# Optimization experiments

Hardware: AMD Instinct MI355X
Metric: run time of the kernel (lower is better)

## Reference

```python
import jax, jax.numpy as jnp
import numpy as np

N_POS = 8192
BATCH = 4
N_GT = 512
EPS = 1e-6
P_EXP = -1.0  # generalized-mean exponent (p < 0)


def setup_inputs() -> dict:
    key = jax.random.key(0)
    k1, k2, k3 = jax.random.split(key, 3)
    dis_matrix = jax.random.uniform(k1, (N_POS, N_POS), dtype=jnp.float32)
    prob_map = jax.random.uniform(k2, (BATCH, N_POS), dtype=jnp.float32)
    gt = jax.random.randint(k3, (BATCH, N_GT), 0, N_POS, dtype=jnp.int64 if jax.config.jax_enable_x64 else jnp.int32)
    return {"prob_map": prob_map, "gt": gt, "dis_matrix": dis_matrix}


def reference(prob_map, gt, dis_matrix):
    max_dist = jnp.max(dis_matrix)
    # global min-max normalization with detached min/range (matches torch .detach())
    pmin = jax.lax.stop_gradient(jnp.min(prob_map))
    prange = jax.lax.stop_gradient(jnp.max(prob_map) - jnp.min(prob_map))
    prob = jnp.clip((prob_map - pmin) / prange, 0.0, 1.0)  # (B, N)

    # gather gt-indexed columns: dis_matrix[:, gt] -> (N, B, G) -> (B, N, G)
    D = jnp.transpose(jnp.take(dis_matrix, gt, axis=1), (1, 0, 2))

    n_est = prob.sum(axis=1)  # (B,)
    # term 1: (1/n_est) * sum_n p_n * min_g D[n, g]
    term1 = jnp.sum(prob * jnp.min(D, axis=2), axis=1) / (n_est + EPS)  # (B,)

    # term 2: generalized mean over pixel dim of weighted distance matrix
    w = (1.0 - prob)[:, :, None] * max_dist + prob[:, :, None] * D  # (B, N, G)
    minn = jnp.mean((w + EPS) ** P_EXP, axis=1) ** (1.0 / P_EXP)  # (B, G)
    term2 = jnp.mean(minn, axis=1)  # (B,)

    return jnp.mean(term1) + jnp.mean(term2)
```

## Files before the change

### kernel.cpp

```cpp
#include <hip/hip_runtime.h>
#include <math.h>

#define N_POS 8192
#define BATCH 4
#define N_GT 512
#define BG 2048
#define EPSV 1e-6f

#define KA_BLOCKS 2048
#define ROWS_A 4
#define KC_BLOCKS 1024
#define ROWS_C 8
#define RG 32
#define CHUNKS_PER_RG (KC_BLOCKS / RG)

#define WS_DPACK 0
#define WS_PARTS (N_POS * BG)
#define WS_PARTS2 (WS_PARTS + KC_BLOCKS * BG)
#define WS_MIND  (WS_PARTS2 + RG * BG)
#define WS_MAXP  (WS_MIND + BATCH * N_POS)
#define WS_SC    (WS_MAXP + KA_BLOCKS)

__global__ __launch_bounds__(256) void whd_kA(const float* __restrict__ dis,
                                              const int* __restrict__ gt,
                                              float* __restrict__ wsf) {
    __shared__ float rowbuf[N_POS];
    __shared__ unsigned short gtl[BG];
    __shared__ float smax[4];
    const int t = threadIdx.x;
    const int wv = t >> 6, lane = t & 63;
    const int row0 = blockIdx.x * ROWS_A;
    float* dpack = wsf + WS_DPACK;
    float* minD = wsf + WS_MIND;

    for (int i = t; i < BG; i += 256) gtl[i] = (unsigned short)gt[i];
    __syncthreads();
    int c[8];
    #pragma unroll
    for (int k = 0; k < 8; k++) c[k] = gtl[8 * t + k];

    float tmax = -INFINITY;
    for (int r = 0; r < ROWS_A; r++) {
        const int n = row0 + r;
        if (r > 0) __syncthreads();
        const float4* src = (const float4*)(dis + (size_t)n * N_POS);
        float4* dstl = (float4*)rowbuf;
        #pragma unroll
        for (int j = 0; j < N_POS / 4 / 256; j++) {
            int i = t + 256 * j;
            float4 v = src[i];
            tmax = fmaxf(tmax, fmaxf(fmaxf(v.x, v.y), fmaxf(v.z, v.w)));
            dstl[i] = v;
        }
        __syncthreads();
        float g0 = rowbuf[c[0]], g1 = rowbuf[c[1]], g2 = rowbuf[c[2]], g3 = rowbuf[c[3]];
        float g4 = rowbuf[c[4]], g5 = rowbuf[c[5]], g6 = rowbuf[c[6]], g7 = rowbuf[c[7]];
        float4* dst = (float4*)(dpack + (size_t)n * BG + 8 * t);
        dst[0] = make_float4(g0, g1, g2, g3);
        dst[1] = make_float4(g4, g5, g6, g7);
        float m = fminf(fminf(fminf(g0, g1), fminf(g2, g3)),
                        fminf(fminf(g4, g5), fminf(g6, g7)));
        #pragma unroll
        for (int off = 32; off; off >>= 1) m = fminf(m, __shfl_xor(m, off, 64));
        if (lane == 0) minD[wv * N_POS + n] = m;
    }
    #pragma unroll
    for (int off = 32; off; off >>= 1) tmax = fmaxf(tmax, __shfl_down(tmax, off, 64));
    if (lane == 0) smax[wv] = tmax;
    __syncthreads();
    if (t == 0)
        wsf[WS_MAXP + blockIdx.x] = fmaxf(fmaxf(smax[0], smax[1]), fmaxf(smax[2], smax[3]));
}

__global__ __launch_bounds__(1024) void whd_kB(const float* __restrict__ prob,
                                               float* __restrict__ wsf) {
    __shared__ float red[1024];
    const int t = threadIdx.x;
    float m = -INFINITY;
    for (int i = t; i < KA_BLOCKS; i += 1024) m = fmaxf(m, wsf[WS_MAXP + i]);
    red[t] = m; __syncthreads();
    for (int s = 512; s; s >>= 1) { if (t < s) red[t] = fmaxf(red[t], red[t + s]); __syncthreads(); }
    float maxdist = red[0]; __syncthreads();
    float lmin = INFINITY, lmax = -INFINITY;
    for (int i = t; i < BATCH * N_POS; i += 1024) {
        float v = prob[i];
        lmin = fminf(lmin, v); lmax = fmaxf(lmax, v);
    }
    red[t] = lmin; __syncthreads();
    for (int s = 512; s; s >>= 1) { if (t < s) red[t] = fminf(red[t], red[t + s]); __syncthreads(); }
    float pmin = red[0]; __syncthreads();
    red[t] = lmax; __syncthreads();
    for (int s = 512; s; s >>= 1) { if (t < s) red[t] = fmaxf(red[t], red[t + s]); __syncthreads(); }
    float pmax = red[0]; __syncthreads();
    float invr = 1.0f / (pmax - pmin);
    const float* minD = wsf + WS_MIND;
    for (int b = 0; b < BATCH; b++) {
        float sp = 0.f, spm = 0.f;
        for (int i = t; i < N_POS; i += 1024) {
            float p = (prob[b * N_POS + i] - pmin) * invr;
            p = fminf(fmaxf(p, 0.f), 1.f);
            sp += p;
            spm += p * minD[b * N_POS + i];
        }
        red[t] = sp; __syncthreads();
        for (int s = 512; s; s >>= 1) { if (t < s) red[t] += red[t + s]; __syncthreads(); }
        if (t == 0) wsf[WS_SC + 3 + b] = red[0];
        __syncthreads();
        red[t] = spm; __syncthreads();
        for (int s = 512; s; s >>= 1) { if (t < s) red[t] += red[t + s]; __syncthreads(); }
        if (t == 0) wsf[WS_SC + 7 + b] = red[0];
        __syncthreads();
    }
    if (t == 0) {
        wsf[WS_SC + 0] = maxdist;
        wsf[WS_SC + 1] = pmin;
        wsf[WS_SC + 2] = pmax - pmin;
        wsf[WS_SC + 11] = 0.f;
    }
}

__global__ __launch_bounds__(256) void whd_kC(const float* __restrict__ prob,
                                              float* __restrict__ wsf) {
    const int t = threadIdx.x;
    const int wv = t >> 6;
    const int row0 = blockIdx.x * ROWS_C;
    const float* dpack = wsf + WS_DPACK;
    const float maxd = wsf[WS_SC + 0];
    const float pmin = wsf[WS_SC + 1];
    const float invr = 1.0f / wsf[WS_SC + 2];
    float acc[8];
    #pragma unroll
    for (int k = 0; k < 8; k++) acc[k] = 0.f;
    #pragma unroll
    for (int r = 0; r < ROWS_C; r++) {
        const int n = row0 + r;
        float p = (prob[wv * N_POS + n] - pmin) * invr;
        p = fminf(fmaxf(p, 0.f), 1.f);
        const float4* rp = (const float4*)(dpack + (size_t)n * BG + 8 * t);
        float4 v0 = rp[0], v1 = rp[1];
        acc[0] += 1.0f / (fmaf(p, v0.x - maxd, maxd) + EPSV);
        acc[1] += 1.0f / (fmaf(p, v0.y - maxd, maxd) + EPSV);
        acc[2] += 1.0f / (fmaf(p, v0.z - maxd, maxd) + EPSV);
        acc[3] += 1.0f / (fmaf(p, v0.w - maxd, maxd) + EPSV);
        acc[4] += 1.0f / (fmaf(p, v1.x - maxd, maxd) + EPSV);
        acc[5] += 1.0f / (fmaf(p, v1.y - maxd, maxd) + EPSV);
        acc[6] += 1.0f / (fmaf(p, v1.z - maxd, maxd) + EPSV);
        acc[7] += 1.0f / (fmaf(p, v1.w - maxd, maxd) + EPSV);
    }
    float4* op = (float4*)(wsf + WS_PARTS + (size_t)blockIdx.x * BG + 8 * t);
    op[0] = make_float4(acc[0], acc[1], acc[2], acc[3]);
    op[1] = make_float4(acc[4], acc[5], acc[6], acc[7]);
}

__global__ __launch_bounds__(256) void whd_kD1(float* __restrict__ wsf) {
    const int t = threadIdx.x;
    const int col = blockIdx.x * 256 + t;
    const int rg = blockIdx.y;
    const float* parts = wsf + WS_PARTS + (size_t)rg * CHUNKS_PER_RG * BG;
    float s = 0.f;
    #pragma unroll 8
    for (int ch = 0; ch < CHUNKS_PER_RG; ch++) s += parts[(size_t)ch * BG + col];
    wsf[WS_PARTS2 + (size_t)rg * BG + col] = s;
}

__global__ __launch_bounds__(256) void whd_kD2(float* __restrict__ wsf) {
    __shared__ float red[256];
    const int t = threadIdx.x;
    const int col = blockIdx.x * 256 + t;
    const float* p2 = wsf + WS_PARTS2;
    float s = 0.f;
    #pragma unroll
    for (int rg = 0; rg < RG; rg++) s += p2[(size_t)rg * BG + col];
    float val = (float)N_POS / s;
    red[t] = val; __syncthreads();
    for (int st = 128; st; st >>= 1) { if (t < st) red[t] += red[t + st]; __syncthreads(); }
    if (t == 0) atomicAdd(&wsf[WS_SC + 11], red[0]);
}

__global__ __launch_bounds__(64) void whd_kE(const float* __restrict__ wsf,
                                             float* __restrict__ out) {
    if (threadIdx.x == 0) {
        float term1 = 0.f;
        for (int b = 0; b < BATCH; b++)
            term1 += wsf[WS_SC + 7 + b] / (wsf[WS_SC + 3 + b] + EPSV);
        term1 *= (1.0f / BATCH);
        float term2 = wsf[WS_SC + 11] * (1.0f / BG);
        out[0] = term1 + term2;
    }
}

extern "C" void kernel_launch(void* const* d_in, const int* in_sizes, int n_in,
                              void* d_out, int out_size, void* d_ws, size_t ws_size,
                              hipStream_t stream) {
    const float* prob = (const float*)d_in[0];
    const int* gt = (const int*)d_in[1];
    const float* dis = (const float*)d_in[2];
    float* out = (float*)d_out;
    float* wsf = (float*)d_ws;

    whd_kA<<<KA_BLOCKS, 256, 0, stream>>>(dis, gt, wsf);
    whd_kB<<<1, 1024, 0, stream>>>(prob, wsf);
    whd_kC<<<KC_BLOCKS, 256, 0, stream>>>(prob, wsf);
    whd_kD1<<<dim3(BG / 256, RG), 256, 0, stream>>>(wsf);
    whd_kD2<<<BG / 256, 256, 0, stream>>>(wsf);
    whd_kE<<<1, 64, 0, stream>>>(wsf, out);
}
```

Baseline: 431.5 us.

## Prefetch rows in register, use wave-shuffle reductions, fuse final kernel

The gather kernel now handles 8 rows per block and prefetches the next distance row into registers with nontemporal loads while the current row is processed from shared memory. The scalar-stats kernel replaces shared-memory tree reductions with wave shuffles and vectorised loads. The final kernel is merged into the last reduction using a last-block-done atomic counter, and the packed reads in the accumulation kernel are made nontemporal. This targets latency in the memory-bound row pass and removes launch and barrier overhead, at the cost of more registers and half as many gather blocks.

```diff
diff --git a/kernel.cpp b/kernel.cpp
--- a/kernel.cpp
+++ b/kernel.cpp
@@ -7,8 +7,8 @@
 #define BG 2048
 #define EPSV 1e-6f
 
-#define KA_BLOCKS 2048
-#define ROWS_A 4
+#define KA_BLOCKS 1024
+#define ROWS_A 8
 #define KC_BLOCKS 1024
 #define ROWS_C 8
 #define RG 32
@@ -21,6 +21,8 @@
 #define WS_MAXP  (WS_MIND + BATCH * N_POS)
 #define WS_SC    (WS_MAXP + KA_BLOCKS)
 
+typedef __attribute__((ext_vector_type(4))) float f32x4;
+
 __global__ __launch_bounds__(256) void whd_kA(const float* __restrict__ dis,
                                               const int* __restrict__ gt,
                                               float* __restrict__ wsf) {
@@ -34,6 +36,13 @@
     float* minD = wsf + WS_MIND;
 
     for (int i = t; i < BG; i += 256) gtl[i] = (unsigned short)gt[i];
+
+    f32x4 pre[8];
+    {
+        const f32x4* src = (const f32x4*)(dis + (size_t)row0 * N_POS);
+        #pragma unroll
+        for (int j = 0; j < 8; j++) pre[j] = __builtin_nontemporal_load(src + t + 256 * j);
+    }
     __syncthreads();
     int c[8];
     #pragma unroll
@@ -42,27 +51,32 @@
     float tmax = -INFINITY;
     for (int r = 0; r < ROWS_A; r++) {
         const int n = row0 + r;
-        if (r > 0) __syncthreads();
-        const float4* src = (const float4*)(dis + (size_t)n * N_POS);
-        float4* dstl = (float4*)rowbuf;
-        #pragma unroll
-        for (int j = 0; j < N_POS / 4 / 256; j++) {
-            int i = t + 256 * j;
-            float4 v = src[i];
+        f32x4* dstl = (f32x4*)rowbuf;
+        #pragma unroll
+        for (int j = 0; j < 8; j++) {
+            f32x4 v = pre[j];
             tmax = fmaxf(tmax, fmaxf(fmaxf(v.x, v.y), fmaxf(v.z, v.w)));
-            dstl[i] = v;
+            dstl[t + 256 * j] = v;
+        }
+        if (r + 1 < ROWS_A) {
+            const f32x4* srcn = (const f32x4*)(dis + (size_t)(n + 1) * N_POS);
+            #pragma unroll
+            for (int j = 0; j < 8; j++) pre[j] = __builtin_nontemporal_load(srcn + t + 256 * j);
         }
         __syncthreads();
         float g0 = rowbuf[c[0]], g1 = rowbuf[c[1]], g2 = rowbuf[c[2]], g3 = rowbuf[c[3]];
         float g4 = rowbuf[c[4]], g5 = rowbuf[c[5]], g6 = rowbuf[c[6]], g7 = rowbuf[c[7]];
-        float4* dst = (float4*)(dpack + (size_t)n * BG + 8 * t);
-        dst[0] = make_float4(g0, g1, g2, g3);
-        dst[1] = make_float4(g4, g5, g6, g7);
+        f32x4* dst = (f32x4*)(dpack + (size_t)n * BG + 8 * t);
+        f32x4 pk0; pk0.x = g0; pk0.y = g1; pk0.z = g2; pk0.w = g3;
+        f32x4 pk1; pk1.x = g4; pk1.y = g5; pk1.z = g6; pk1.w = g7;
+        dst[0] = pk0;
+        dst[1] = pk1;
         float m = fminf(fminf(fminf(g0, g1), fminf(g2, g3)),
                         fminf(fminf(g4, g5), fminf(g6, g7)));
         #pragma unroll
         for (int off = 32; off; off >>= 1) m = fminf(m, __shfl_xor(m, off, 64));
         if (lane == 0) minD[wv * N_POS + n] = m;
+        if (r + 1 < ROWS_A) __syncthreads();
     }
     #pragma unroll
     for (int off = 32; off; off >>= 1) tmax = fmaxf(tmax, __shfl_down(tmax, off, 64));
@@ -74,48 +88,71 @@
 
 __global__ __launch_bounds__(1024) void whd_kB(const float* __restrict__ prob,
                                                float* __restrict__ wsf) {
-    __shared__ float red[1024];
-    const int t = threadIdx.x;
+    __shared__ float sA[16], sB[16], sC[16];
+    const int t = threadIdx.x, wv = t >> 6, lane = t & 63;
+
     float m = -INFINITY;
     for (int i = t; i < KA_BLOCKS; i += 1024) m = fmaxf(m, wsf[WS_MAXP + i]);
-    red[t] = m; __syncthreads();
-    for (int s = 512; s; s >>= 1) { if (t < s) red[t] = fmaxf(red[t], red[t + s]); __syncthreads(); }
-    float maxdist = red[0]; __syncthreads();
+    #pragma unroll
+    for (int off = 32; off; off >>= 1) m = fmaxf(m, __shfl_xor(m, off, 64));
+
     float lmin = INFINITY, lmax = -INFINITY;
-    for (int i = t; i < BATCH * N_POS; i += 1024) {
-        float v = prob[i];
-        lmin = fminf(lmin, v); lmax = fmaxf(lmax, v);
-    }
-    red[t] = lmin; __syncthreads();
-    for (int s = 512; s; s >>= 1) { if (t < s) red[t] = fminf(red[t], red[t + s]); __syncthreads(); }
-    float pmin = red[0]; __syncthreads();
-    red[t] = lmax; __syncthreads();
-    for (int s = 512; s; s >>= 1) { if (t < s) red[t] = fmaxf(red[t], red[t + s]); __syncthreads(); }
-    float pmax = red[0]; __syncthreads();
-    float invr = 1.0f / (pmax - pmin);
-    const float* minD = wsf + WS_MIND;
+    const f32x4* p4 = (const f32x4*)prob;
+    for (int i = t; i < BATCH * N_POS / 4; i += 1024) {
+        f32x4 v = p4[i];
+        lmin = fminf(fminf(lmin, fminf(v.x, v.y)), fminf(v.z, v.w));
+        lmax = fmaxf(fmaxf(lmax, fmaxf(v.x, v.y)), fmaxf(v.z, v.w));
+    }
+    #pragma unroll
+    for (int off = 32; off; off >>= 1) {
+        lmin = fminf(lmin, __shfl_xor(lmin, off, 64));
+        lmax = fmaxf(lmax, __shfl_xor(lmax, off, 64));
+    }
+    if (lane == 0) { sA[wv] = m; sB[wv] = lmin; sC[wv] = lmax; }
+    __syncthreads();
+    if (t == 0) {
+        float maxd = -INFINITY, mn = INFINITY, mx = -INFINITY;
+        #pragma unroll
+        for (int i = 0; i < 16; i++) {
+            maxd = fmaxf(maxd, sA[i]); mn = fminf(mn, sB[i]); mx = fmaxf(mx, sC[i]);
+        }
+        wsf[WS_SC + 0] = maxd;
+        wsf[WS_SC + 1] = mn;
+        wsf[WS_SC + 2] = mx - mn;
+        wsf[WS_SC + 11] = 0.f;
+        wsf[WS_SC + 12] = 0.f;
+        sB[0] = mn; sC[0] = 1.0f / (mx - mn);
+    }
+    __syncthreads();
+    const float pmin = sB[0], invr = sC[0];
+
+    const f32x4* d4 = (const f32x4*)(wsf + WS_MIND);
     for (int b = 0; b < BATCH; b++) {
         float sp = 0.f, spm = 0.f;
-        for (int i = t; i < N_POS; i += 1024) {
-            float p = (prob[b * N_POS + i] - pmin) * invr;
-            p = fminf(fmaxf(p, 0.f), 1.f);
-            sp += p;
-            spm += p * minD[b * N_POS + i];
-        }
-        red[t] = sp; __syncthreads();
-        for (int s = 512; s; s >>= 1) { if (t < s) red[t] += red[t + s]; __syncthreads(); }
-        if (t == 0) wsf[WS_SC + 3 + b] = red[0];
+        for (int i = t; i < N_POS / 4; i += 1024) {
+            f32x4 v = p4[b * (N_POS / 4) + i];
+            f32x4 dm = d4[b * (N_POS / 4) + i];
+            float p;
+            p = fminf(fmaxf((v.x - pmin) * invr, 0.f), 1.f); sp += p; spm += p * dm.x;
+            p = fminf(fmaxf((v.y - pmin) * invr, 0.f), 1.f); sp += p; spm += p * dm.y;
+            p = fminf(fmaxf((v.z - pmin) * invr, 0.f), 1.f); sp += p; spm += p * dm.z;
+            p = fminf(fmaxf((v.w - pmin) * invr, 0.f), 1.f); sp += p; spm += p * dm.w;
+        }
+        #pragma unroll
+        for (int off = 32; off; off >>= 1) {
+            sp += __shfl_xor(sp, off, 64);
+            spm += __shfl_xor(spm, off, 64);
+        }
         __syncthreads();
-        red[t] = spm; __syncthreads();
-        for (int s = 512; s; s >>= 1) { if (t < s) red[t] += red[t + s]; __syncthreads(); }
-        if (t == 0) wsf[WS_SC + 7 + b] = red[0];
+        if (lane == 0) { sA[wv] = sp; sB[wv] = spm; }
         __syncthreads();
-    }
-    if (t == 0) {
-        wsf[WS_SC + 0] = maxdist;
-        wsf[WS_SC + 1] = pmin;
-        wsf[WS_SC + 2] = pmax - pmin;
-        wsf[WS_SC + 11] = 0.f;
+        if (t == 0) {
+            float a = 0.f, c2 = 0.f;
+            #pragma unroll
+            for (int i = 0; i < 16; i++) { a += sA[i]; c2 += sB[i]; }
+            wsf[WS_SC + 3 + b] = a;
+            wsf[WS_SC + 7 + b] = c2;
+        }
     }
 }
 
@@ -136,8 +173,9 @@
         const int n = row0 + r;
         float p = (prob[wv * N_POS + n] - pmin) * invr;
         p = fminf(fmaxf(p, 0.f), 1.f);
-        const float4* rp = (const float4*)(dpack + (size_t)n * BG + 8 * t);
-        float4 v0 = rp[0], v1 = rp[1];
+        const f32x4* rp = (const f32x4*)(dpack + (size_t)n * BG + 8 * t);
+        f32x4 v0 = __builtin_nontemporal_load(rp);
+        f32x4 v1 = __builtin_nontemporal_load(rp + 1);
         acc[0] += 1.0f / (fmaf(p, v0.x - maxd, maxd) + EPSV);
         acc[1] += 1.0f / (fmaf(p, v0.y - maxd, maxd) + EPSV);
         acc[2] += 1.0f / (fmaf(p, v0.z - maxd, maxd) + EPSV);
@@ -147,9 +185,11 @@
         acc[6] += 1.0f / (fmaf(p, v1.z - maxd, maxd) + EPSV);
         acc[7] += 1.0f / (fmaf(p, v1.w - maxd, maxd) + EPSV);
     }
-    float4* op = (float4*)(wsf + WS_PARTS + (size_t)blockIdx.x * BG + 8 * t);
-    op[0] = make_float4(acc[0], acc[1], acc[2], acc[3]);
-    op[1] = make_float4(acc[4], acc[5], acc[6], acc[7]);
+    f32x4* op = (f32x4*)(wsf + WS_PARTS + (size_t)blockIdx.x * BG + 8 * t);
+    f32x4 o0; o0.x = acc[0]; o0.y = acc[1]; o0.z = acc[2]; o0.w = acc[3];
+    f32x4 o1; o1.x = acc[4]; o1.y = acc[5]; o1.z = acc[6]; o1.w = acc[7];
+    op[0] = o0;
+    op[1] = o1;
 }
 
 __global__ __launch_bounds__(256) void whd_kD1(float* __restrict__ wsf) {
@@ -163,8 +203,9 @@
     wsf[WS_PARTS2 + (size_t)rg * BG + col] = s;
 }
 
-__global__ __launch_bounds__(256) void whd_kD2(float* __restrict__ wsf) {
-    __shared__ float red[256];
+__global__ __launch_bounds__(256) void whd_kD2(float* __restrict__ wsf,
+                                               float* __restrict__ out) {
+    __shared__ float red[4];
     const int t = threadIdx.x;
     const int col = blockIdx.x * 256 + t;
     const float* p2 = wsf + WS_PARTS2;
@@ -172,20 +213,23 @@
     #pragma unroll
     for (int rg = 0; rg < RG; rg++) s += p2[(size_t)rg * BG + col];
     float val = (float)N_POS / s;
-    red[t] = val; __syncthreads();
-    for (int st = 128; st; st >>= 1) { if (t < st) red[t] += red[t + st]; __syncthreads(); }
-    if (t == 0) atomicAdd(&wsf[WS_SC + 11], red[0]);
-}
-
-__global__ __launch_bounds__(64) void whd_kE(const float* __restrict__ wsf,
-                                             float* __restrict__ out) {
-    if (threadIdx.x == 0) {
-        float term1 = 0.f;
-        for (int b = 0; b < BATCH; b++)
-            term1 += wsf[WS_SC + 7 + b] / (wsf[WS_SC + 3 + b] + EPSV);
-        term1 *= (1.0f / BATCH);
-        float term2 = wsf[WS_SC + 11] * (1.0f / BG);
-        out[0] = term1 + term2;
+    #pragma unroll
+    for (int off = 32; off; off >>= 1) val += __shfl_xor(val, off, 64);
+    if ((t & 63) == 0) red[t >> 6] = val;
+    __syncthreads();
+    if (t == 0) {
+        float blocksum = red[0] + red[1] + red[2] + red[3];
+        atomicAdd(&wsf[WS_SC + 11], blocksum);
+        __threadfence();
+        unsigned prev = atomicAdd((unsigned*)(wsf + WS_SC + 12), 1u);
+        if (prev == gridDim.x - 1) {
+            float t2sum = atomicAdd(&wsf[WS_SC + 11], 0.0f);
+            float term1 = 0.f;
+            #pragma unroll
+            for (int b = 0; b < BATCH; b++)
+                term1 += wsf[WS_SC + 7 + b] / (wsf[WS_SC + 3 + b] + EPSV);
+            out[0] = term1 * (1.0f / BATCH) + t2sum * (1.0f / BG);
+        }
     }
 }
 
@@ -202,6 +246,5 @@
     whd_kB<<<1, 1024, 0, stream>>>(prob, wsf);
     whd_kC<<<KC_BLOCKS, 256, 0, stream>>>(prob, wsf);
     whd_kD1<<<dim3(BG / 256, RG), 256, 0, stream>>>(wsf);
-    whd_kD2<<<BG / 256, 256, 0, stream>>>(wsf);
-    whd_kE<<<1, 64, 0, stream>>>(wsf, out);
-}
+    whd_kD2<<<BG / 256, 256, 0, stream>>>(wsf, out);
+}
```

After: 398.9 us. -7.6%, faster.
